# Kernel tuning notes

Measured on AMD Instinct MI355X. Metric: run time of the kernel, lower is better.

The kernel has to match this reference:

```python
import jax, jax.numpy as jnp
import numpy as np
from jax import lax

B, C, IMG, P = 64, 3, 256, 16
D, K, NC, NH = 128, 512, 8, 4
GRID = IMG // P
N = GRID * GRID  # 256 patches
HD = D // NH


def setup_inputs() -> dict:
    key = jax.random.key(0)
    ks = jax.random.split(key, 16)
    s = 0.02
    f32 = jnp.float32
    return {
        'image': jax.random.uniform(ks[0], (B, C, IMG, IMG), f32),
        'conv_w': jax.random.normal(ks[1], (D, C, P, P), f32) * s,
        'conv_b': jnp.zeros((D,), f32),
        'stat_w1': jax.random.normal(ks[2], (128, 15), f32) * s,
        'stat_b1': jnp.zeros((128,), f32),
        'stat_w2': jax.random.normal(ks[3], (D, 128), f32) * s,
        'stat_b2': jnp.zeros((D,), f32),
        'pos_embed': jax.random.normal(ks[4], (1, N, D), f32) * s,
        'ln1_s': jnp.ones((2, D), f32), 'ln1_b': jnp.zeros((2, D), f32),
        'qkv_w': jax.random.normal(ks[5], (2, 3 * D, D), f32) * s,
        'qkv_b': jnp.zeros((2, 3 * D), f32),
        'out_w': jax.random.normal(ks[6], (2, D, D), f32) * s,
        'out_b': jnp.zeros((2, D), f32),
        'ln2_s': jnp.ones((2, D), f32), 'ln2_b': jnp.zeros((2, D), f32),
        'ff1_w': jax.random.normal(ks[7], (2, 2 * D, D), f32) * s,
        'ff1_b': jnp.zeros((2, 2 * D), f32),
        'ff2_w': jax.random.normal(ks[8], (2, D, 2 * D), f32) * s,
        'ff2_b': jnp.zeros((2, D), f32),
        'codebook': jax.random.uniform(ks[9], (K, D), f32, -1.0 / K, 1.0 / K),
        'head_w': jax.random.normal(ks[10], (NC, D), f32) * s,
        'head_b': jnp.zeros((NC,), f32),
    }


def _ln(x, s, b, eps=1e-5):
    mu = x.mean(-1, keepdims=True)
    var = jnp.var(x, axis=-1, keepdims=True)
    return (x - mu) / jnp.sqrt(var + eps) * s + b


def _stats(image):
    # mean/std(unbiased)/min/max per channel + skew/kurt/dark of luminance -> 15 feats
    px = image.reshape(B, C, -1)
    mean = px.mean(-1)
    std = px.std(-1, ddof=1)
    mn = px.min(-1)
    mx = px.max(-1)
    lum = 0.299 * px[:, 0] + 0.587 * px[:, 1] + 0.114 * px[:, 2]
    cen = lum - lum.mean(-1, keepdims=True)
    sd = lum.std(-1)  # biased, matches unbiased=False
    skew = (cen ** 3).mean(-1) / (sd ** 3 + 1e-6)
    kurt = (cen ** 4).mean(-1) / (sd ** 4 + 1e-6)
    dark = (lum < 0.2).astype(jnp.float32).mean(-1)
    return jnp.concatenate([mean, std, mn, mx, skew[:, None], kurt[:, None], dark[:, None]], -1)


def _forward(image, conv_w, conv_b, stat_w1, stat_b1, stat_w2, stat_b2, pos_embed,
             ln1_s, ln1_b, qkv_w, qkv_b, out_w, out_b, ln2_s, ln2_b,
             ff1_w, ff1_b, ff2_w, ff2_b, codebook, head_w, head_b):
    # patch embedding: non-overlapping conv, stride = kernel = P
    patch = lax.conv_general_dilated(image, conv_w, (P, P), 'VALID',
                                     dimension_numbers=('NCHW', 'OIHW', 'NCHW'))
    patch = (patch + conv_b[None, :, None, None]).reshape(B, D, N).transpose(0, 2, 1)  # (B,N,D)
    # statistical encoder (eval: dropout off)
    sf = jax.nn.relu(_stats(image) @ stat_w1.T + stat_b1) @ stat_w2.T + stat_b2  # (B,D)
    x = patch + pos_embed + sf[:, None, :]
    # 2-layer pre-LN transformer encoder
    for i in range(2):
        h = _ln(x, ln1_s[i], ln1_b[i])
        qkv = h @ qkv_w[i].T + qkv_b[i]
        q, k, v = jnp.split(qkv, 3, axis=-1)
        q = q.reshape(B, N, NH, HD).transpose(0, 2, 1, 3)
        k = k.reshape(B, N, NH, HD).transpose(0, 2, 1, 3)
        v = v.reshape(B, N, NH, HD).transpose(0, 2, 1, 3)
        attn = jax.nn.softmax(jnp.einsum('bhqd,bhkd->bhqk', q, k) / jnp.sqrt(jnp.float32(HD)), -1)
        o = jnp.einsum('bhqk,bhkd->bhqd', attn, v).transpose(0, 2, 1, 3).reshape(B, N, D)
        x = x + o @ out_w[i].T + out_b[i]
        h = _ln(x, ln2_s[i], ln2_b[i])
        x = x + jax.nn.gelu(h @ ff1_w[i].T + ff1_b[i], approximate=False) @ ff2_w[i].T + ff2_b[i]
    # VQ: nearest-codebook lookup with straight-through estimator
    zf = x.reshape(-1, D)
    dist = (zf * zf).sum(1, keepdims=True) + (codebook * codebook).sum(1) - 2.0 * (zf @ codebook.T)
    idx = jnp.argmin(dist, axis=1)  # (B*N,)
    qz = codebook[idx].reshape(B, N, D)
    quant = x + lax.stop_gradient(qz - x)
    counts = jnp.zeros((K,), jnp.float32).at[idx].add(1.0)
    p = counts / idx.size
    perplexity = jnp.exp(-jnp.sum(p * jnp.log(p + 1e-10)))
    gf = quant.mean(1)
    logits = gf @ head_w.T + head_b
    return quant, idx.reshape(B, N), logits, gf, perplexity


def reference(image, conv_w, conv_b, stat_w1, stat_b1, stat_w2, stat_b2, pos_embed,
              ln1_s, ln1_b, qkv_w, qkv_b, out_w, out_b, ln2_s, ln2_b,
              ff1_w, ff1_b, ff2_w, ff2_b, codebook, head_w, head_b):
    return _forward(image, conv_w, conv_b, stat_w1, stat_b1, stat_w2, stat_b2, pos_embed,
                    ln1_s, ln1_b, qkv_w, qkv_b, out_w, out_b, ln2_s, ln2_b,
                    ff1_w, ff1_b, ff2_w, ff2_b, codebook, head_w, head_b)
```

## Files before the change

kernel.cpp:

```cpp
#include <hip/hip_runtime.h>
#include <math.h>

__device__ __forceinline__ double wred_add(double v) {
    #pragma unroll
    for (int o = 32; o > 0; o >>= 1) v += __shfl_xor(v, o);
    return v;
}
__device__ __forceinline__ float wred_min(float v) {
    #pragma unroll
    for (int o = 32; o > 0; o >>= 1) v = fminf(v, __shfl_xor(v, o));
    return v;
}
__device__ __forceinline__ float wred_max(float v) {
    #pragma unroll
    for (int o = 32; o > 0; o >>= 1) v = fmaxf(v, __shfl_xor(v, o));
    return v;
}

#define PREC 17

__global__ __launch_bounds__(256) void stats_partial_kernel(const float* __restrict__ img,
                                                            double* __restrict__ part)
{
    int b = blockIdx.x >> 5, blk = blockIdx.x & 31;
    int tid = threadIdx.x;
    const float* r0 = img + (size_t)b * 3 * 65536;
    const float* g0 = r0 + 65536;
    const float* b0 = r0 + 131072;
    int base = blk*2048 + tid*8;
    double s0=0,s1=0,s2=0,q0=0,q1=0,q2=0,l1=0,l2=0,l3=0,l4=0,dark=0;
    float mn0=1e30f,mn1=1e30f,mn2=1e30f, mx0=-1e30f,mx1=-1e30f,mx2=-1e30f;
    #pragma unroll
    for (int u = 0; u < 2; ++u) {
        float4 rv = *(const float4*)&r0[base + u*4];
        float4 gv = *(const float4*)&g0[base + u*4];
        float4 bv = *(const float4*)&b0[base + u*4];
        float rr[4] = {rv.x, rv.y, rv.z, rv.w};
        float gg[4] = {gv.x, gv.y, gv.z, gv.w};
        float bbv[4] = {bv.x, bv.y, bv.z, bv.w};
        #pragma unroll
        for (int e = 0; e < 4; ++e) {
            float r = rr[e], g = gg[e], bl = bbv[e];
            double rd_ = r, gd = g, bd = bl;
            s0 += rd_; q0 += rd_*rd_; mn0 = fminf(mn0, r); mx0 = fmaxf(mx0, r);
            s1 += gd;  q1 += gd*gd;   mn1 = fminf(mn1, g); mx1 = fmaxf(mx1, g);
            s2 += bd;  q2 += bd*bd;   mn2 = fminf(mn2, bl); mx2 = fmaxf(mx2, bl);
            double lum = 0.299*rd_ + 0.587*gd + 0.114*bd;
            double d2 = lum*lum;
            l1 += lum; l2 += d2; l3 += d2*lum; l4 += d2*d2;
            if (lum < 0.2) dark += 1.0;
        }
    }
    double dv[11] = {s0,s1,s2,q0,q1,q2,l1,l2,l3,l4,dark};
    #pragma unroll
    for (int q = 0; q < 11; ++q) dv[q] = wred_add(dv[q]);
    mn0 = wred_min(mn0); mn1 = wred_min(mn1); mn2 = wred_min(mn2);
    mx0 = wred_max(mx0); mx1 = wred_max(mx1); mx2 = wred_max(mx2);
    __shared__ double sd[4][PREC];
    int w = tid >> 6, lane = tid & 63;
    if (lane == 0) {
        #pragma unroll
        for (int q = 0; q < 11; ++q) sd[w][q] = dv[q];
        sd[w][11] = (double)mn0; sd[w][12] = (double)mn1; sd[w][13] = (double)mn2;
        sd[w][14] = (double)mx0; sd[w][15] = (double)mx1; sd[w][16] = (double)mx2;
    }
    __syncthreads();
    if (tid == 0) {
        double out[PREC];
        #pragma unroll
        for (int q = 0; q < PREC; ++q) out[q] = sd[0][q];
        #pragma unroll
        for (int ww = 1; ww < 4; ++ww) {
            #pragma unroll
            for (int q = 0; q < 11; ++q) out[q] += sd[ww][q];
            out[11] = fmin(out[11], sd[ww][11]); out[12] = fmin(out[12], sd[ww][12]);
            out[13] = fmin(out[13], sd[ww][13]);
            out[14] = fmax(out[14], sd[ww][14]); out[15] = fmax(out[15], sd[ww][15]);
            out[16] = fmax(out[16], sd[ww][16]);
        }
        double* p = part + (size_t)(b*32 + blk)*PREC;
        #pragma unroll
        for (int q = 0; q < PREC; ++q) p[q] = out[q];
    }
}

__global__ __launch_bounds__(32) void stats_final_kernel(const double* __restrict__ part,
                                                         double* __restrict__ feats)
{
    int b = blockIdx.x, t = threadIdx.x;
    const double* p = part + (size_t)(b*32 + t)*PREC;
    double v[PREC];
    #pragma unroll
    for (int q = 0; q < PREC; ++q) v[q] = p[q];
    #pragma unroll
    for (int o = 16; o > 0; o >>= 1) {
        #pragma unroll
        for (int q = 0; q < 11; ++q) v[q] += __shfl_xor(v[q], o);
        #pragma unroll
        for (int q = 11; q < 14; ++q) v[q] = fmin(v[q], __shfl_xor(v[q], o));
        #pragma unroll
        for (int q = 14; q < PREC; ++q) v[q] = fmax(v[q], __shfl_xor(v[q], o));
    }
    if (t == 0) {
        const double n = 65536.0;
        double* f = feats + b*15;
        for (int c = 0; c < 3; ++c) {
            double su = v[c], sq = v[3+c];
            f[c]   = su/n;
            f[3+c] = sqrt((sq - su*su/n) / (n - 1.0));
            f[6+c] = v[11+c];
            f[9+c] = v[14+c];
        }
        double m1 = v[6]/n, m2 = v[7]/n, m3 = v[8]/n, m4 = v[9]/n;
        double mu2 = m2 - m1*m1;
        double mu3 = m3 - 3.0*m1*m2 + 2.0*m1*m1*m1;
        double mu4 = m4 - 4.0*m1*m3 + 6.0*m1*m1*m2 - 3.0*m1*m1*m1*m1;
        double sd = sqrt(mu2);
        f[12] = mu3 / (sd*sd*sd + 1e-6);
        f[13] = mu4 / (sd*sd*sd*sd + 1e-6);
        f[14] = v[10] / n;
    }
}

__global__ __launch_bounds__(128) void sfmlp_kernel(const double* __restrict__ feats,
    const float* __restrict__ w1, const float* __restrict__ b1,
    const float* __restrict__ w2, const float* __restrict__ b2,
    double* __restrict__ sf)
{
    int b = blockIdx.x, t = threadIdx.x;
    __shared__ double fs[15];
    __shared__ double hs[128];
    if (t < 15) fs[t] = feats[b*15 + t];
    __syncthreads();
    double h = (double)b1[t];
    for (int j = 0; j < 15; ++j) h += fs[j] * (double)w1[t*15 + j];
    hs[t] = fmax(h, 0.0);
    __syncthreads();
    double o = (double)b2[t];
    for (int j = 0; j < 128; ++j) o += hs[j] * (double)w2[t*128 + j];
    sf[b*128 + t] = o;
}

__device__ __forceinline__ int swz64(int r, int kq4) {
    return r*64 + (((kq4) ^ (r & 15)) << 2);
}

__global__ __launch_bounds__(256) void patch_gemm_kernel(const float* __restrict__ img,
    const float* __restrict__ w, const float* __restrict__ bias,
    const float* __restrict__ pos, const double* __restrict__ sf,
    float* __restrict__ xout)
{
    __shared__ float As[4096];
    __shared__ float Ws[4096];
    int tid = threadIdx.x;
    int tx = tid & 15, ty = tid >> 4;
    int m0 = blockIdx.x * 64, n0 = blockIdx.y * 64;
    int kq = tid & 15;
    int r0 = tid >> 4;
    float acc[4][4] = {};
    for (int k0 = 0; k0 < 768; k0 += 64) {
        #pragma unroll
        for (int p = 0; p < 4; ++p) {
            int row = p*16 + r0;
            int m = m0 + row;
            int bb = m >> 8, pat = m & 255;
            int gy = pat >> 4, gx = pat & 15;
            int k = k0 + kq*4;
            int c = k >> 8, rem = k & 255;
            int py = rem >> 4, px = rem & 15;
            float4 av = *(const float4*)&img[(size_t)(bb*3 + c)*65536 + (size_t)(gy*16+py)*256 + gx*16 + px];
            *(float4*)&As[swz64(row, kq)] = av;
            float4 wv = *(const float4*)&w[(size_t)(n0+row)*768 + k];
            *(float4*)&Ws[swz64(row, kq)] = wv;
        }
        __syncthreads();
        #pragma unroll 8
        for (int q = 0; q < 16; ++q) {
            float4 a4[4], w4[4];
            #pragma unroll
            for (int i=0;i<4;++i) a4[i] = *(const float4*)&As[swz64(ty + 16*i, q)];
            #pragma unroll
            for (int j=0;j<4;++j) w4[j] = *(const float4*)&Ws[swz64(tx + 16*j, q)];
            #pragma unroll
            for (int i=0;i<4;++i)
                #pragma unroll
                for (int j=0;j<4;++j) {
                    acc[i][j] = fmaf(a4[i].x, w4[j].x, acc[i][j]);
                    acc[i][j] = fmaf(a4[i].y, w4[j].y, acc[i][j]);
                    acc[i][j] = fmaf(a4[i].z, w4[j].z, acc[i][j]);
                    acc[i][j] = fmaf(a4[i].w, w4[j].w, acc[i][j]);
                }
        }
        __syncthreads();
    }
    #pragma unroll
    for (int i=0;i<4;++i){
        int m = m0 + ty + 16*i;
        int bb = m >> 8, pat = m & 255;
        #pragma unroll
        for (int j=0;j<4;++j){
            int n = n0 + tx + 16*j;
            float v = acc[i][j] + bias[n];
            v += pos[pat*128 + n];
            v += (float)sf[bb*128 + n];
            xout[(size_t)m*128 + n] = v;
        }
    }
}

__global__ __launch_bounds__(256) void ln_kernel(const float* __restrict__ x,
    const float* __restrict__ s, const float* __restrict__ bta, float* __restrict__ out)
{
    int tid = threadIdx.x;
    int lane = tid & 63, w = tid >> 6;
    int row = blockIdx.x*4 + w;
    float2 v = *(const float2*)&x[(size_t)row*128 + lane*2];
    double v0 = v.x, v1 = v.y;
    double sum = v0 + v1, sq = v0*v0 + v1*v1;
    #pragma unroll
    for (int o = 32; o > 0; o >>= 1) { sum += __shfl_xor(sum, o); sq += __shfl_xor(sq, o); }
    double mean = sum * (1.0/128.0);
    double var  = sq  * (1.0/128.0) - mean*mean;
    double inv  = 1.0 / sqrt(var + 1e-5);
    float2 o2;
    o2.x = (float)((v0 - mean)*inv*(double)s[lane*2]   + (double)bta[lane*2]);
    o2.y = (float)((v1 - mean)*inv*(double)s[lane*2+1] + (double)bta[lane*2+1]);
    *(float2*)&out[(size_t)row*128 + lane*2] = o2;
}

__global__ __launch_bounds__(256) void gemm_kernel(const float* __restrict__ A, int lda,
    const float* __restrict__ W, const float* __restrict__ bias,
    float* __restrict__ C, float* __restrict__ Xres,
    int M, int N, int K, int epi)
{
    __shared__ float As[4096];
    __shared__ float Ws[4096];
    int tid = threadIdx.x;
    int tx = tid & 15, ty = tid >> 4;
    int m0 = blockIdx.x * 64, n0 = blockIdx.y * 64;
    int kq = tid & 15;
    int r0 = tid >> 4;
    float acc[4][4] = {};
    for (int k0 = 0; k0 < K; k0 += 64) {
        #pragma unroll
        for (int p = 0; p < 4; ++p) {
            int row = p*16 + r0;
            float4 av = *(const float4*)&A[(size_t)(m0+row)*lda + k0 + kq*4];
            *(float4*)&As[swz64(row, kq)] = av;
            float4 wv = *(const float4*)&W[(size_t)(n0+row)*K + k0 + kq*4];
            *(float4*)&Ws[swz64(row, kq)] = wv;
        }
        __syncthreads();
        #pragma unroll 8
        for (int q = 0; q < 16; ++q) {
            float4 a4[4], w4[4];
            #pragma unroll
            for (int i=0;i<4;++i) a4[i] = *(const float4*)&As[swz64(ty + 16*i, q)];
            #pragma unroll
            for (int j=0;j<4;++j) w4[j] = *(const float4*)&Ws[swz64(tx + 16*j, q)];
            #pragma unroll
            for (int i=0;i<4;++i)
                #pragma unroll
                for (int j=0;j<4;++j) {
                    acc[i][j] = fmaf(a4[i].x, w4[j].x, acc[i][j]);
                    acc[i][j] = fmaf(a4[i].y, w4[j].y, acc[i][j]);
                    acc[i][j] = fmaf(a4[i].z, w4[j].z, acc[i][j]);
                    acc[i][j] = fmaf(a4[i].w, w4[j].w, acc[i][j]);
                }
        }
        __syncthreads();
    }
    #pragma unroll
    for (int i=0;i<4;++i){
        int m = m0 + ty + 16*i;
        #pragma unroll
        for (int j=0;j<4;++j){
            int n = n0 + tx + 16*j;
            float v = acc[i][j] + bias[n];
            if (epi == 0) {
                C[(size_t)m*N + n] = v;
            } else if (epi == 1) {
                Xres[(size_t)m*N + n] += v;
            } else {
                C[(size_t)m*N + n] = 0.5f*v*(1.0f + erff(v*0.70710678118654752f));
            }
        }
    }
}

__global__ __launch_bounds__(1024) void attn_kernel(float* __restrict__ qkv)
{
    __shared__ float Ks[256*36];
    __shared__ float Vs[256*36];
    int tid = threadIdx.x;
    int b = blockIdx.x >> 2, h = blockIdx.x & 3;
    int qrow = tid >> 2;
    int ksec = tid & 3;
    {
        size_t rb = (size_t)(b*256 + qrow) * 384;
        const float* kp = qkv + rb + 128 + h*32 + ksec*8;
        const float* vp = qkv + rb + 256 + h*32 + ksec*8;
        *(float4*)&Ks[qrow*36 + ksec*8]     = *(const float4*)&kp[0];
        *(float4*)&Ks[qrow*36 + ksec*8 + 4] = *(const float4*)&kp[4];
        *(float4*)&Vs[qrow*36 + ksec*8]     = *(const float4*)&vp[0];
        *(float4*)&Vs[qrow*36 + ksec*8 + 4] = *(const float4*)&vp[4];
    }
    float q[32];
    const float* qp = qkv + (size_t)(b*256 + qrow)*384 + h*32;
    #pragma unroll
    for (int i = 0; i < 32; ++i) q[i] = qp[i];
    __syncthreads();
    float o[32];
    #pragma unroll
    for (int i = 0; i < 32; ++i) o[i] = 0.f;
    float m = -INFINITY, l = 0.f;
    const float scale = 0.17677669529663687f;
    for (int it = 0; it < 64; ++it) {
        int j = it*4 + ksec;
        const float* kr = &Ks[j*36];
        float s = 0.f;
        #pragma unroll
        for (int i = 0; i < 32; ++i) s = fmaf(q[i], kr[i], s);
        s *= scale;
        const float* vr = &Vs[j*36];
        if (__all(s <= m)) {
            float e = expf(s - m);
            l += e;
            #pragma unroll
            for (int i = 0; i < 32; ++i) o[i] = fmaf(e, vr[i], o[i]);
        } else {
            float mn = fmaxf(m, s);
            float f = expf(m - mn);
            float e = expf(s - mn);
            l = l*f + e;
            #pragma unroll
            for (int i = 0; i < 32; ++i) o[i] = fmaf(o[i], f, e*vr[i]);
            m = mn;
        }
    }
    #pragma unroll
    for (int off = 1; off <= 2; off <<= 1) {
        float mo = __shfl_xor(m, off);
        float lo = __shfl_xor(l, off);
        float M  = fmaxf(m, mo);
        float ea = expf(m - M), eb = expf(mo - M);
        l = l*ea + lo*eb;
        #pragma unroll
        for (int i = 0; i < 32; ++i) {
            float oo = __shfl_xor(o[i], off);
            o[i] = o[i]*ea + oo*eb;
        }
        m = M;
    }
    if (ksec == 0) {
        float inv = 1.0f / l;
        float* op = qkv + (size_t)(b*256 + qrow)*384 + h*32;
        #pragma unroll
        for (int i = 0; i < 32; ++i) op[i] = o[i] * inv;
    }
}

__global__ __launch_bounds__(256) void cc_kernel(const float* __restrict__ cb,
                                                 float* __restrict__ ccs)
{
    int c = blockIdx.x*256 + threadIdx.x;
    const float* p = cb + (size_t)c*128;
    float r[8];
    #pragma unroll
    for (int j = 0; j < 8; ++j) { float v = p[j]; r[j] = v*v; }
    for (int i = 8; i < 128; i += 8)
        #pragma unroll
        for (int j = 0; j < 8; ++j) { float v = p[i+j]; r[j] += v*v; }
    ccs[c] = ((r[0]+r[1]) + (r[2]+r[3])) + ((r[4]+r[5]) + (r[6]+r[7]));
}

#define ZC(k) (((k)&3)==0 ? z[(k)>>2].x : ((k)&3)==1 ? z[(k)>>2].y : ((k)&3)==2 ? z[(k)>>2].z : z[(k)>>2].w)

__global__ __launch_bounds__(128) void vq_dist_kernel(const float* __restrict__ x,
    const float* __restrict__ cb, const float* __restrict__ ccs,
    float* __restrict__ pbv, int* __restrict__ pbi)
{
    __shared__ float Cs[8192];
    __shared__ float ccl[64];
    int tid = threadIdx.x;
    int m = blockIdx.x*128 + tid;
    int split = blockIdx.y;
    int cbase = split*64;
    const float4* cbp = (const float4*)(cb + (size_t)cbase*128);
    for (int e = tid; e < 2048; e += 128) ((float4*)Cs)[e] = cbp[e];
    if (tid < 64) ccl[tid] = ccs[cbase + tid];
    float4 z[32];
    const float4* zp = (const float4*)(x + (size_t)m*128);
    #pragma unroll
    for (int i = 0; i < 32; ++i) z[i] = zp[i];
    float r[8];
    #pragma unroll
    for (int j = 0; j < 8; ++j) { float v = ZC(j); r[j] = v*v; }
    #pragma unroll
    for (int i = 8; i < 128; i += 8)
        #pragma unroll
        for (int j = 0; j < 8; ++j) { float v = ZC(i+j); r[j] += v*v; }
    float zz = ((r[0]+r[1]) + (r[2]+r[3])) + ((r[4]+r[5]) + (r[6]+r[7]));
    __syncthreads();
    float bestv = INFINITY;
    int   besti = 0;
    for (int g = 0; g < 16; ++g) {
        const float* c0 = &Cs[(g*4+0)*128];
        const float* c1 = &Cs[(g*4+1)*128];
        const float* c2 = &Cs[(g*4+2)*128];
        const float* c3 = &Cs[(g*4+3)*128];
        float a0 = 0.f, a1 = 0.f, a2 = 0.f, a3 = 0.f;
        #pragma unroll
        for (int q = 0; q < 32; ++q) {
            float4 v0 = *(const float4*)&c0[q*4];
            float4 v1 = *(const float4*)&c1[q*4];
            float4 v2 = *(const float4*)&c2[q*4];
            float4 v3 = *(const float4*)&c3[q*4];
            float4 zq = z[q];
            a0 = fmaf(zq.x, v0.x, a0); a0 = fmaf(zq.y, v0.y, a0);
            a0 = fmaf(zq.z, v0.z, a0); a0 = fmaf(zq.w, v0.w, a0);
            a1 = fmaf(zq.x, v1.x, a1); a1 = fmaf(zq.y, v1.y, a1);
            a1 = fmaf(zq.z, v1.z, a1); a1 = fmaf(zq.w, v1.w, a1);
            a2 = fmaf(zq.x, v2.x, a2); a2 = fmaf(zq.y, v2.y, a2);
            a2 = fmaf(zq.z, v2.z, a2); a2 = fmaf(zq.w, v2.w, a2);
            a3 = fmaf(zq.x, v3.x, a3); a3 = fmaf(zq.y, v3.y, a3);
            a3 = fmaf(zq.z, v3.z, a3); a3 = fmaf(zq.w, v3.w, a3);
        }
        int code = cbase + g*4;
        float t1, d;
        t1 = zz + ccl[g*4+0]; d = t1 - 2.0f*a0; if (d < bestv) { bestv = d; besti = code;   }
        t1 = zz + ccl[g*4+1]; d = t1 - 2.0f*a1; if (d < bestv) { bestv = d; besti = code+1; }
        t1 = zz + ccl[g*4+2]; d = t1 - 2.0f*a2; if (d < bestv) { bestv = d; besti = code+2; }
        t1 = zz + ccl[g*4+3]; d = t1 - 2.0f*a3; if (d < bestv) { bestv = d; besti = code+3; }
    }
    pbv[(size_t)split*16384 + m] = bestv;
    pbi[(size_t)split*16384 + m] = besti;
}

__global__ __launch_bounds__(256) void vq_merge_kernel(const float* __restrict__ pbv,
    const int* __restrict__ pbi, const float* __restrict__ cb,
    float* __restrict__ quant, float* __restrict__ idxf, float* __restrict__ counts)
{
    __shared__ int fidx[256];
    int tid = threadIdx.x;
    int m0 = blockIdx.x*256;
    int m = m0 + tid;
    float v = pbv[m]; int gi = pbi[m];
    #pragma unroll
    for (int s = 1; s < 8; ++s) {
        float vv = pbv[(size_t)s*16384 + m]; int ii = pbi[(size_t)s*16384 + m];
        if (vv < v) { v = vv; gi = ii; }
    }
    fidx[tid] = gi;
    idxf[m] = (float)gi;
    atomicAdd(&counts[gi], 1.0f);
    __syncthreads();
    for (int e = tid; e < 8192; e += 256) {
        int rr = e >> 5, k4 = e & 31;
        ((float4*)&quant[(size_t)(m0+rr)*128])[k4] = ((const float4*)&cb[(size_t)fidx[rr]*128])[k4];
    }
}

__global__ __launch_bounds__(128) void gf_logits_kernel(const float* __restrict__ quant,
    const float* __restrict__ head_w, const float* __restrict__ head_b,
    float* __restrict__ gf, float* __restrict__ logits)
{
    int b = blockIdx.x, d = threadIdx.x;
    double s = 0.0;
    for (int n = 0; n < 256; ++n) s += (double)quant[(size_t)(b*256+n)*128 + d];
    double g = s * (1.0/256.0);
    gf[b*128 + d] = (float)g;
    __shared__ double gs[128];
    gs[d] = g;
    __syncthreads();
    if (d < 8) {
        double l = (double)head_b[d];
        for (int k = 0; k < 128; ++k) l += gs[k] * (double)head_w[d*128 + k];
        logits[b*8 + d] = (float)l;
    }
}

__global__ __launch_bounds__(512) void perp_kernel(const float* __restrict__ counts,
                                                   float* __restrict__ out)
{
    __shared__ double sh[512];
    int t = threadIdx.x;
    double p = (double)counts[t] * (1.0/16384.0);
    sh[t] = p * log(p + 1e-10);
    __syncthreads();
    for (int s = 256; s > 0; s >>= 1) { if (t < s) sh[t] += sh[t+s]; __syncthreads(); }
    if (t == 0) out[0] = (float)exp(-sh[0]);
}

extern "C" void kernel_launch(void* const* d_in, const int* in_sizes, int n_in,
                              void* d_out, int out_size, void* d_ws, size_t ws_size,
                              hipStream_t stream)
{
    const float* image   = (const float*)d_in[0];
    const float* conv_w  = (const float*)d_in[1];
    const float* conv_b  = (const float*)d_in[2];
    const float* stat_w1 = (const float*)d_in[3];
    const float* stat_b1 = (const float*)d_in[4];
    const float* stat_w2 = (const float*)d_in[5];
    const float* stat_b2 = (const float*)d_in[6];
    const float* pos     = (const float*)d_in[7];
    const float* ln1_s   = (const float*)d_in[8];
    const float* ln1_b   = (const float*)d_in[9];
    const float* qkv_w   = (const float*)d_in[10];
    const float* qkv_b   = (const float*)d_in[11];
    const float* out_w   = (const float*)d_in[12];
    const float* out_b   = (const float*)d_in[13];
    const float* ln2_s   = (const float*)d_in[14];
    const float* ln2_b   = (const float*)d_in[15];
    const float* ff1_w   = (const float*)d_in[16];
    const float* ff1_b   = (const float*)d_in[17];
    const float* ff2_w   = (const float*)d_in[18];
    const float* ff2_b   = (const float*)d_in[19];
    const float* codebook= (const float*)d_in[20];
    const float* head_w  = (const float*)d_in[21];
    const float* head_b  = (const float*)d_in[22];

    char* wsb = (char*)d_ws;
    float*  x32   = (float*) (wsb);
    float*  h32   = (float*) (wsb + 8388608);
    float*  qkv32 = (float*) (wsb + 16777216);
    double* sf64  = (double*)(wsb + 41943040);
    double* feats = (double*)(wsb + 42008576);
    float*  counts= (float*) (wsb + 42016256);
    double* part  = (double*)(wsb + 42018304);
    float*  pbv   = (float*) (wsb + 42296832);
    int*    pbi   = (int*)   (wsb + 42821120);
    float*  ccs   = (float*) (wsb + 43345408);

    float* outf   = (float*)d_out;
    float* quant  = outf;
    float* idxf   = quant + 2097152;
    float* logits = idxf + 16384;
    float* gf     = logits + 512;
    float* perp   = gf + 8192;

    hipMemsetAsync(counts, 0, 512*sizeof(float), stream);

    stats_partial_kernel<<<2048, 256, 0, stream>>>(image, part);
    stats_final_kernel<<<64, 32, 0, stream>>>(part, feats);
    sfmlp_kernel<<<64, 128, 0, stream>>>(feats, stat_w1, stat_b1, stat_w2, stat_b2, sf64);
    patch_gemm_kernel<<<dim3(256, 2), 256, 0, stream>>>(image, conv_w, conv_b, pos, sf64, x32);
    cc_kernel<<<2, 256, 0, stream>>>(codebook, ccs);

    for (int i = 0; i < 2; ++i) {
        ln_kernel<<<4096, 256, 0, stream>>>(x32, ln1_s + i*128, ln1_b + i*128, h32);
        gemm_kernel<<<dim3(256, 6), 256, 0, stream>>>(h32, 128, qkv_w + (size_t)i*384*128,
                                                      qkv_b + i*384, qkv32, nullptr,
                                                      16384, 384, 128, 0);
        attn_kernel<<<256, 1024, 0, stream>>>(qkv32);
        gemm_kernel<<<dim3(256, 2), 256, 0, stream>>>(qkv32, 384, out_w + (size_t)i*128*128,
                                                      out_b + i*128, nullptr, x32,
                                                      16384, 128, 128, 1);
        ln_kernel<<<4096, 256, 0, stream>>>(x32, ln2_s + i*128, ln2_b + i*128, h32);
        gemm_kernel<<<dim3(256, 4), 256, 0, stream>>>(h32, 128, ff1_w + (size_t)i*256*128,
                                                      ff1_b + i*256, qkv32, nullptr,
                                                      16384, 256, 128, 2);
        gemm_kernel<<<dim3(256, 2), 256, 0, stream>>>(qkv32, 256, ff2_w + (size_t)i*128*256,
                                                      ff2_b + i*128, nullptr, x32,
                                                      16384, 128, 256, 1);
    }

    vq_dist_kernel<<<dim3(128, 8), 128, 0, stream>>>(x32, codebook, ccs, pbv, pbi);
    vq_merge_kernel<<<64, 256, 0, stream>>>(pbv, pbi, codebook, quant, idxf, counts);
    gf_logits_kernel<<<64, 128, 0, stream>>>(quant, head_w, head_b, gf, logits);
    perp_kernel<<<1, 512, 0, stream>>>(counts, perp);
}
```

Baseline: 549.5 us.

## Split-K the N=128 GEMMs and fuse bias, residual and LayerNorm reductions

The patch-embedding, attention-output and FF2 GEMMs, which each launched only 512 blocks, now split K into two halves across blockIdx.z. This doubles the block count, and each half writes its partial sums to scratch buffers. New reduction kernels sum the partials and add bias, position and stat features or the residual, then apply the following LayerNorm in the same pass, so the standalone LN kernels go away. In exchange, extra partial buffers are written and read back, and the scratch aliasing inside the qkv buffer and h32 must not collide.

```diff
diff --git a/kernel.cpp b/kernel.cpp
--- a/kernel.cpp
+++ b/kernel.cpp
@@ -145,33 +145,31 @@
     return r*64 + (((kq4) ^ (r & 15)) << 2);
 }
 
-__global__ __launch_bounds__(256) void patch_gemm_kernel(const float* __restrict__ img,
-    const float* __restrict__ w, const float* __restrict__ bias,
-    const float* __restrict__ pos, const double* __restrict__ sf,
-    float* __restrict__ xout)
+__global__ __launch_bounds__(256) void patch_sk_kernel(const float* __restrict__ img,
+    const float* __restrict__ w, float* __restrict__ P0, float* __restrict__ P1)
 {
     __shared__ float As[4096];
     __shared__ float Ws[4096];
     int tid = threadIdx.x;
     int tx = tid & 15, ty = tid >> 4;
     int m0 = blockIdx.x * 64, n0 = blockIdx.y * 64;
+    int kbase = blockIdx.z * 384;
     int kq = tid & 15;
     int r0 = tid >> 4;
     float acc[4][4] = {};
-    for (int k0 = 0; k0 < 768; k0 += 64) {
+    for (int k0 = 0; k0 < 384; k0 += 64) {
         #pragma unroll
         for (int p = 0; p < 4; ++p) {
             int row = p*16 + r0;
             int m = m0 + row;
             int bb = m >> 8, pat = m & 255;
             int gy = pat >> 4, gx = pat & 15;
-            int k = k0 + kq*4;
+            int k = kbase + k0 + kq*4;
             int c = k >> 8, rem = k & 255;
             int py = rem >> 4, px = rem & 15;
-            float4 av = *(const float4*)&img[(size_t)(bb*3 + c)*65536 + (size_t)(gy*16+py)*256 + gx*16 + px];
-            *(float4*)&As[swz64(row, kq)] = av;
-            float4 wv = *(const float4*)&w[(size_t)(n0+row)*768 + k];
-            *(float4*)&Ws[swz64(row, kq)] = wv;
+            *(float4*)&As[swz64(row, kq)] =
+                *(const float4*)&img[(size_t)(bb*3 + c)*65536 + (size_t)(gy*16+py)*256 + gx*16 + px];
+            *(float4*)&Ws[swz64(row, kq)] = *(const float4*)&w[(size_t)(n0+row)*768 + k];
         }
         __syncthreads();
         #pragma unroll 8
@@ -193,45 +191,21 @@
         }
         __syncthreads();
     }
+    float* P = blockIdx.z ? P1 : P0;
     #pragma unroll
     for (int i=0;i<4;++i){
         int m = m0 + ty + 16*i;
-        int bb = m >> 8, pat = m & 255;
         #pragma unroll
         for (int j=0;j<4;++j){
             int n = n0 + tx + 16*j;
-            float v = acc[i][j] + bias[n];
-            v += pos[pat*128 + n];
-            v += (float)sf[bb*128 + n];
-            xout[(size_t)m*128 + n] = v;
-        }
-    }
-}
-
-__global__ __launch_bounds__(256) void ln_kernel(const float* __restrict__ x,
-    const float* __restrict__ s, const float* __restrict__ bta, float* __restrict__ out)
-{
-    int tid = threadIdx.x;
-    int lane = tid & 63, w = tid >> 6;
-    int row = blockIdx.x*4 + w;
-    float2 v = *(const float2*)&x[(size_t)row*128 + lane*2];
-    double v0 = v.x, v1 = v.y;
-    double sum = v0 + v1, sq = v0*v0 + v1*v1;
-    #pragma unroll
-    for (int o = 32; o > 0; o >>= 1) { sum += __shfl_xor(sum, o); sq += __shfl_xor(sq, o); }
-    double mean = sum * (1.0/128.0);
-    double var  = sq  * (1.0/128.0) - mean*mean;
-    double inv  = 1.0 / sqrt(var + 1e-5);
-    float2 o2;
-    o2.x = (float)((v0 - mean)*inv*(double)s[lane*2]   + (double)bta[lane*2]);
-    o2.y = (float)((v1 - mean)*inv*(double)s[lane*2+1] + (double)bta[lane*2+1]);
-    *(float2*)&out[(size_t)row*128 + lane*2] = o2;
+            P[(size_t)m*128 + n] = acc[i][j];
+        }
+    }
 }
 
 __global__ __launch_bounds__(256) void gemm_kernel(const float* __restrict__ A, int lda,
     const float* __restrict__ W, const float* __restrict__ bias,
-    float* __restrict__ C, float* __restrict__ Xres,
-    int M, int N, int K, int epi)
+    float* __restrict__ C, int M, int N, int K, int epi)
 {
     __shared__ float As[4096];
     __shared__ float Ws[4096];
@@ -245,10 +219,8 @@
         #pragma unroll
         for (int p = 0; p < 4; ++p) {
             int row = p*16 + r0;
-            float4 av = *(const float4*)&A[(size_t)(m0+row)*lda + k0 + kq*4];
-            *(float4*)&As[swz64(row, kq)] = av;
-            float4 wv = *(const float4*)&W[(size_t)(n0+row)*K + k0 + kq*4];
-            *(float4*)&Ws[swz64(row, kq)] = wv;
+            *(float4*)&As[swz64(row, kq)] = *(const float4*)&A[(size_t)(m0+row)*lda + k0 + kq*4];
+            *(float4*)&Ws[swz64(row, kq)] = *(const float4*)&W[(size_t)(n0+row)*K + k0 + kq*4];
         }
         __syncthreads();
         #pragma unroll 8
@@ -279,12 +251,122 @@
             float v = acc[i][j] + bias[n];
             if (epi == 0) {
                 C[(size_t)m*N + n] = v;
-            } else if (epi == 1) {
-                Xres[(size_t)m*N + n] += v;
             } else {
                 C[(size_t)m*N + n] = 0.5f*v*(1.0f + erff(v*0.70710678118654752f));
             }
         }
+    }
+}
+
+__global__ __launch_bounds__(256) void gemm_sk_kernel(const float* __restrict__ A, int lda,
+    const float* __restrict__ W, int K, int K2,
+    float* __restrict__ P0, float* __restrict__ P1, int ldo)
+{
+    __shared__ float As[4096];
+    __shared__ float Ws[4096];
+    int tid = threadIdx.x;
+    int tx = tid & 15, ty = tid >> 4;
+    int m0 = blockIdx.x * 64, n0 = blockIdx.y * 64;
+    int kbase = blockIdx.z * K2;
+    int kq = tid & 15;
+    int r0 = tid >> 4;
+    float acc[4][4] = {};
+    for (int k0 = 0; k0 < K2; k0 += 64) {
+        #pragma unroll
+        for (int p = 0; p < 4; ++p) {
+            int row = p*16 + r0;
+            *(float4*)&As[swz64(row, kq)] = *(const float4*)&A[(size_t)(m0+row)*lda + kbase + k0 + kq*4];
+            *(float4*)&Ws[swz64(row, kq)] = *(const float4*)&W[(size_t)(n0+row)*K + kbase + k0 + kq*4];
+        }
+        __syncthreads();
+        #pragma unroll 8
+        for (int q = 0; q < 16; ++q) {
+            float4 a4[4], w4[4];
+            #pragma unroll
+            for (int i=0;i<4;++i) a4[i] = *(const float4*)&As[swz64(ty + 16*i, q)];
+            #pragma unroll
+            for (int j=0;j<4;++j) w4[j] = *(const float4*)&Ws[swz64(tx + 16*j, q)];
+            #pragma unroll
+            for (int i=0;i<4;++i)
+                #pragma unroll
+                for (int j=0;j<4;++j) {
+                    acc[i][j] = fmaf(a4[i].x, w4[j].x, acc[i][j]);
+                    acc[i][j] = fmaf(a4[i].y, w4[j].y, acc[i][j]);
+                    acc[i][j] = fmaf(a4[i].z, w4[j].z, acc[i][j]);
+                    acc[i][j] = fmaf(a4[i].w, w4[j].w, acc[i][j]);
+                }
+        }
+        __syncthreads();
+    }
+    float* P = blockIdx.z ? P1 : P0;
+    #pragma unroll
+    for (int i=0;i<4;++i){
+        int m = m0 + ty + 16*i;
+        #pragma unroll
+        for (int j=0;j<4;++j){
+            int n = n0 + tx + 16*j;
+            P[(size_t)m*ldo + n] = acc[i][j];
+        }
+    }
+}
+
+__global__ __launch_bounds__(256) void cpatch_kernel(const float* __restrict__ p0,
+    const float* __restrict__ p1, const float* __restrict__ bias,
+    const float* __restrict__ pos, const double* __restrict__ sf,
+    const float* __restrict__ ls, const float* __restrict__ lb,
+    float* __restrict__ x, float* __restrict__ h)
+{
+    int tid = threadIdx.x;
+    int lane = tid & 63, w = tid >> 6;
+    int row = blockIdx.x*4 + w;
+    int bb = row >> 8, pat = row & 255;
+    int n = lane*2;
+    float2 a0 = *(const float2*)&p0[(size_t)row*128 + n];
+    float2 a1 = *(const float2*)&p1[(size_t)row*128 + n];
+    float v0 = a0.x + a1.x + bias[n]   + pos[pat*128 + n]   + (float)sf[bb*128 + n];
+    float v1 = a0.y + a1.y + bias[n+1] + pos[pat*128 + n+1] + (float)sf[bb*128 + n+1];
+    *(float2*)&x[(size_t)row*128 + n] = make_float2(v0, v1);
+    double v0d = v0, v1d = v1;
+    double sum = v0d + v1d, sq = v0d*v0d + v1d*v1d;
+    #pragma unroll
+    for (int o = 32; o > 0; o >>= 1) { sum += __shfl_xor(sum, o); sq += __shfl_xor(sq, o); }
+    double mean = sum * (1.0/128.0);
+    double var  = sq  * (1.0/128.0) - mean*mean;
+    double inv  = 1.0 / sqrt(var + 1e-5);
+    float2 o2;
+    o2.x = (float)((v0d - mean)*inv*(double)ls[n]   + (double)lb[n]);
+    o2.y = (float)((v1d - mean)*inv*(double)ls[n+1] + (double)lb[n+1]);
+    *(float2*)&h[(size_t)row*128 + n] = o2;
+}
+
+__global__ __launch_bounds__(256) void cres_kernel(float* __restrict__ x,
+    const float* __restrict__ p0, int ld0, const float* __restrict__ p1, int ld1,
+    const float* __restrict__ bias,
+    const float* __restrict__ ls, const float* __restrict__ lb,
+    float* __restrict__ h, int doLN)
+{
+    int tid = threadIdx.x;
+    int lane = tid & 63, w = tid >> 6;
+    int row = blockIdx.x*4 + w;
+    int n = lane*2;
+    float2 a0 = *(const float2*)&p0[(size_t)row*ld0 + n];
+    float2 a1 = *(const float2*)&p1[(size_t)row*ld1 + n];
+    float2 xv = *(const float2*)&x[(size_t)row*128 + n];
+    float v0 = xv.x + (a0.x + a1.x + bias[n]);
+    float v1 = xv.y + (a0.y + a1.y + bias[n+1]);
+    *(float2*)&x[(size_t)row*128 + n] = make_float2(v0, v1);
+    if (doLN) {
+        double v0d = v0, v1d = v1;
+        double sum = v0d + v1d, sq = v0d*v0d + v1d*v1d;
+        #pragma unroll
+        for (int o = 32; o > 0; o >>= 1) { sum += __shfl_xor(sum, o); sq += __shfl_xor(sq, o); }
+        double mean = sum * (1.0/128.0);
+        double var  = sq  * (1.0/128.0) - mean*mean;
+        double inv  = 1.0 / sqrt(var + 1e-5);
+        float2 o2;
+        o2.x = (float)((v0d - mean)*inv*(double)ls[n]   + (double)lb[n]);
+        o2.y = (float)((v1d - mean)*inv*(double)ls[n+1] + (double)lb[n+1]);
+        *(float2*)&h[(size_t)row*128 + n] = o2;
     }
 }
 
@@ -544,25 +626,31 @@
     stats_partial_kernel<<<2048, 256, 0, stream>>>(image, part);
     stats_final_kernel<<<64, 32, 0, stream>>>(part, feats);
     sfmlp_kernel<<<64, 128, 0, stream>>>(feats, stat_w1, stat_b1, stat_w2, stat_b2, sf64);
-    patch_gemm_kernel<<<dim3(256, 2), 256, 0, stream>>>(image, conv_w, conv_b, pos, sf64, x32);
     cc_kernel<<<2, 256, 0, stream>>>(codebook, ccs);
 
+    patch_sk_kernel<<<dim3(256, 2, 2), 256, 0, stream>>>(image, conv_w,
+                                                         qkv32, qkv32 + 2097152);
+    cpatch_kernel<<<4096, 256, 0, stream>>>(qkv32, qkv32 + 2097152, conv_b, pos, sf64,
+                                            ln1_s, ln1_b, x32, h32);
+
     for (int i = 0; i < 2; ++i) {
-        ln_kernel<<<4096, 256, 0, stream>>>(x32, ln1_s + i*128, ln1_b + i*128, h32);
         gemm_kernel<<<dim3(256, 6), 256, 0, stream>>>(h32, 128, qkv_w + (size_t)i*384*128,
-                                                      qkv_b + i*384, qkv32, nullptr,
-                                                      16384, 384, 128, 0);
+                                                      qkv_b + i*384, qkv32, 16384, 384, 128, 0);
         attn_kernel<<<256, 1024, 0, stream>>>(qkv32);
-        gemm_kernel<<<dim3(256, 2), 256, 0, stream>>>(qkv32, 384, out_w + (size_t)i*128*128,
-                                                      out_b + i*128, nullptr, x32,
-                                                      16384, 128, 128, 1);
-        ln_kernel<<<4096, 256, 0, stream>>>(x32, ln2_s + i*128, ln2_b + i*128, h32);
+        gemm_sk_kernel<<<dim3(256, 2, 2), 256, 0, stream>>>(qkv32, 384,
+                                                            out_w + (size_t)i*128*128, 128, 64,
+                                                            qkv32 + 128, qkv32 + 256, 384);
+        cres_kernel<<<4096, 256, 0, stream>>>(x32, qkv32 + 128, 384, qkv32 + 256, 384,
+                                              out_b + i*128, ln2_s + i*128, ln2_b + i*128,
+                                              h32, 1);
         gemm_kernel<<<dim3(256, 4), 256, 0, stream>>>(h32, 128, ff1_w + (size_t)i*256*128,
-                                                      ff1_b + i*256, qkv32, nullptr,
-                                                      16384, 256, 128, 2);
-        gemm_kernel<<<dim3(256, 2), 256, 0, stream>>>(qkv32, 256, ff2_w + (size_t)i*128*256,
-                                                      ff2_b + i*128, nullptr, x32,
-                                                      16384, 128, 256, 1);
+                                                      ff1_b + i*256, qkv32, 16384, 256, 128, 2);
+        gemm_sk_kernel<<<dim3(256, 2, 2), 256, 0, stream>>>(qkv32, 256,
+                                                            ff2_w + (size_t)i*128*256, 256, 128,
+                                                            qkv32 + 4194304, h32, 128);
+        cres_kernel<<<4096, 256, 0, stream>>>(x32, qkv32 + 4194304, 128, h32, 128,
+                                              ff2_b + i*128, ln1_s + 128, ln1_b + 128,
+                                              h32, i == 0 ? 1 : 0);
     }
 
     vq_dist_kernel<<<dim3(128, 8), 128, 0, stream>>>(x32, codebook, ccs, pbv, pbi);
```

Result: faster. 537.4 us (-2.2%).
